# Kernel optimization log

Measured on AMD Instinct MI355X. Metric: run time of the kernel, lower is better.

The kernel has to match this reference:

```python
import jax, jax.numpy as jnp
import numpy as np

EMBED = 1024
ADIM = 1024
H = 16
HD = ADIM // H          # 64
RAY = 48                # ray_subdim
R = RAY // 3            # 16
SCALE = 1.0 / np.sqrt(HD)
NB = 768                # boundary tokens
MN = 8                  # max neighbors
FG = 6                  # face_group
L = 1024                # tokens per face
B = 12                  # b * face_group
STAGES = 4


def _apply_dray(x, d, einsum_str, inverse):
    ray = x[..., :RAY].reshape(x.shape[:-1] + (3, R))
    if inverse:
        d = jnp.swapaxes(d, -1, -2)
    ray = jnp.einsum(einsum_str, d, ray).reshape(x.shape[:-1] + (RAY,))
    return jnp.concatenate([ray, x[..., RAY:]], axis=-1)


def setup_inputs() -> dict:
    key = jax.random.key(0)
    ks = jax.random.split(key, 12)
    inp = {}
    inp['x'] = jax.random.normal(ks[0], (B, L, EMBED), dtype=jnp.float32)
    inp['qkv_w'] = jax.random.normal(ks[1], (EMBED, 3 * ADIM), dtype=jnp.float32) * 0.02
    inp['out_w'] = jax.random.normal(ks[2], (ADIM, EMBED), dtype=jnp.float32) * 0.02
    inp['out_b'] = jax.random.normal(ks[3], (EMBED,), dtype=jnp.float32) * 0.02
    inp['d_ray'] = jax.random.normal(ks[4], (STAGES, FG, L, 3, 3), dtype=jnp.float32)
    inp['boundary_face_ids'] = jax.random.randint(ks[5], (NB,), 0, FG, dtype=jnp.int32).astype(jnp.int64)
    inp['boundary_token_indices'] = jnp.arange(NB, dtype=jnp.int64)
    inp['boundary_local_indices'] = jax.random.randint(ks[6], (NB,), 0, L, dtype=jnp.int32).astype(jnp.int64)
    inp['boundary_stage_ids'] = jax.random.randint(ks[7], (NB,), 0, STAGES, dtype=jnp.int32).astype(jnp.int64)
    inp['neighbor_face_ids'] = jax.random.randint(ks[8], (NB, MN), 0, FG, dtype=jnp.int32).astype(jnp.int64)
    inp['neighbor_token_indices'] = jax.random.randint(ks[9], (NB, MN), 0, L, dtype=jnp.int32).astype(jnp.int64)
    inp['neighbor_local_indices'] = jax.random.randint(ks[10], (NB, MN), 0, L, dtype=jnp.int32).astype(jnp.int64)
    inp['neighbor_stage_ids'] = jax.random.randint(ks[11], (NB, MN), 0, STAGES, dtype=jnp.int32).astype(jnp.int64)
    inp['neighbor_mask'] = jnp.ones((NB, MN), dtype=bool)
    inp['face_group'] = FG
    return inp


def reference(x, qkv_w, out_w, out_b, d_ray,
              boundary_face_ids, boundary_token_indices, boundary_local_indices, boundary_stage_ids,
              neighbor_face_ids, neighbor_token_indices, neighbor_local_indices, neighbor_stage_ids,
              neighbor_mask, face_group):
    b = x.shape[0] // face_group
    l = x.shape[1]
    xt = x.reshape(b, face_group, l, EMBED)          # [b, FG, L, E]
    max_face, max_idx = face_group - 1, l - 1

    qf = jnp.clip(boundary_face_ids, 0, max_face)
    qi = jnp.clip(boundary_token_indices, 0, max_idx)
    valid_q = (boundary_face_ids == qf) & (boundary_token_indices == qi)

    nf = jnp.clip(neighbor_face_ids, 0, max_face)
    ni = jnp.clip(neighbor_token_indices, 0, max_idx)
    mask = neighbor_mask & (neighbor_face_ids == nf) & (neighbor_token_indices == ni)

    # gather boundary queries and neighbor keys/values
    x_q = xt[:, qf, qi, :]                            # [b, NB, E]
    x_kv = xt[:, nf, ni, :]                           # [b, NB, MN, E]
    q = (x_q @ qkv_w)[..., :ADIM]
    kv = x_kv @ qkv_w
    k = kv[..., ADIM:2 * ADIM]
    v = kv[..., 2 * ADIM:]

    nb, mn = q.shape[1], k.shape[2]
    q = q.reshape(b, nb, H, HD)
    k = k.reshape(b, nb, mn, H, HD)
    v = v.reshape(b, nb, mn, H, HD)

    d_q = d_ray[boundary_stage_ids, boundary_face_ids, boundary_local_indices]     # [NB, 3, 3]
    d_k = d_ray[neighbor_stage_ids,
                jnp.maximum(neighbor_face_ids, 0),
                jnp.maximum(neighbor_local_indices, 0)]                            # [NB, MN, 3, 3]

    q = _apply_dray(q, d_q, 'nij,bnhjr->bnhir', inverse=False)
    k = _apply_dray(k, d_k, 'nmij,bnmhjr->bnmhir', inverse=False)
    v = _apply_dray(v, d_k, 'nmij,bnmhjr->bnmhir', inverse=False)

    attn = jnp.einsum('bnhd,bnmhd->bnmh', q, k) * SCALE
    attn = jnp.where(mask[None, :, :, None], attn, -jnp.inf)
    attn = jax.nn.softmax(attn, axis=2)               # softmax over neighbors
    out = jnp.einsum('bnmh,bnmhd->bnhd', attn, v)

    out = _apply_dray(out, d_q, 'nij,bnhjr->bnhir', inverse=True)
    out = out.reshape(b, nb, ADIM) @ out_w + out_b
    out = out * valid_q[None, :, None].astype(out.dtype)

    out_full = jnp.zeros_like(xt).at[:, qf, qi, :].set(out)
    return out_full.reshape(-1, l, EMBED)
```

## Files before the change

kernel.cpp:

```cpp
#include <hip/hip_runtime.h>
#include <hip/hip_bf16.h>
#include <cstddef>

#define FG 6
#define L 1024
#define NB 768
#define MN 8
#define H 16
#define HD 64
#define ADIM 1024
#define STAGES 4
#define SCALE 0.125f

typedef __attribute__((ext_vector_type(8))) short bf16x8;
typedef __attribute__((ext_vector_type(4))) float f32x4;
typedef __attribute__((address_space(3))) short lds_short_t;
typedef const __attribute__((address_space(1))) short g_short_t;

__device__ __forceinline__ int clampi(int v, int lo, int hi) {
  return v < lo ? lo : (v > hi ? hi : v);
}

__device__ __forceinline__ short f2bf(float f) {
  __hip_bfloat16 h = __float2bfloat16(f);
  return *reinterpret_cast<short*>(&h);
}

__device__ __forceinline__ void gload16(const short* g, short* l) {
  __builtin_amdgcn_global_load_lds((g_short_t*)g, (lds_short_t*)l, 16, 0, 0);
}

__global__ __launch_bounds__(256)
void conv_bf16(const float* __restrict__ in, short* __restrict__ out) {
  size_t i = ((size_t)blockIdx.x * 256 + threadIdx.x) * 8;
  float4 a = *(const float4*)(in + i);
  float4 b = *(const float4*)(in + i + 4);
  bf16x8 v;
  v[0] = f2bf(a.x); v[1] = f2bf(a.y); v[2] = f2bf(a.z); v[3] = f2bf(a.w);
  v[4] = f2bf(b.x); v[5] = f2bf(b.y); v[6] = f2bf(b.z); v[7] = f2bf(b.w);
  *(bf16x8*)(out + i) = v;
}

__global__ __launch_bounds__(256)
void transpose_both(const float* __restrict__ qkv_w, short* __restrict__ qwT,
                    const float* __restrict__ out_w, short* __restrict__ owT) {
  const int z = blockIdx.z;
  if (z == 1 && blockIdx.x >= 32) return;
  const float* in = z ? out_w : qkv_w;
  short* out = z ? owT : qwT;
  const int N = z ? 1024 : 3072;
  __shared__ float tile[32][33];
  const int n0 = blockIdx.x * 32, k0 = blockIdx.y * 32;
  const int tx = threadIdx.x & 31, ty = threadIdx.x >> 5;
  #pragma unroll
  for (int i = 0; i < 4; ++i)
    tile[ty + i * 8][tx] = in[(size_t)(k0 + ty + i * 8) * N + n0 + tx];
  __syncthreads();
  #pragma unroll
  for (int i = 0; i < 4; ++i)
    out[(size_t)(n0 + ty + i * 8) * 1024 + k0 + tx] =
        f2bf(tile[tx][ty + i * 8]);
}

__global__ __launch_bounds__(256)
void q_gemm128(const short* __restrict__ A, const short* __restrict__ B,
               float* __restrict__ C,
               const int* __restrict__ f_ids, const int* __restrict__ t_ids)
{
  __shared__ __align__(16) short As[8192];
  __shared__ __align__(16) short Bs[8192];

  const int tid  = threadIdx.x;
  const int w    = tid >> 6, lane = tid & 63;
  const int row0 = blockIdx.y * 128, col0 = blockIdx.x * 128;

  size_t aoff[4], boff[4];
  short *adst[4], *bdst[4];
  #pragma unroll
  for (int c = 0; c < 4; ++c) {
    const int d = (w * 4 + c) * 64 + lane;
    const int r = d >> 3;
    const int ssrc = (d & 7) ^ (r & 7);
    const int rr = row0 + r;
    const int bi = rr >= NB;
    const int idx = rr - bi * NB;
    const int f = clampi(f_ids[idx], 0, FG - 1);
    const int q = clampi(t_ids[idx], 0, L - 1);
    const long gr = (long)(bi * FG + f) * L + q;
    aoff[c] = (size_t)gr * 1024 + ssrc * 8;
    boff[c] = (size_t)(col0 + r) * 1024 + ssrc * 8;
    adst[c] = As + (w * 4 + c) * 512;
    bdst[c] = Bs + (w * 4 + c) * 512;
  }

  const int lr = lane & 15, lq = lane >> 4;
  const int wrow = (w >> 1) * 64, wcol = (w & 1) * 64;
  const int sA = lr & 7;
  const char* As8 = (const char*)As;
  const char* Bs8 = (const char*)Bs;
  const int abase = (wrow + lr) * 128;
  const int bbase = (wcol + lr) * 128;

  f32x4 acc[4][4];
  #pragma unroll
  for (int m = 0; m < 4; ++m)
    #pragma unroll
    for (int n = 0; n < 4; ++n) acc[m][n] = (f32x4){0.f, 0.f, 0.f, 0.f};

  for (int kt = 0; kt < 16; ++kt) {
    #pragma unroll
    for (int c = 0; c < 4; ++c) {
      gload16(A + aoff[c] + kt * 64, adst[c]);
      gload16(B + boff[c] + kt * 64, bdst[c]);
    }
    __syncthreads();
    #pragma unroll
    for (int kk = 0; kk < 2; ++kk) {
      const int so = ((kk * 4 + lq) ^ sA) << 4;
      bf16x8 av[4], bv[4];
      #pragma unroll
      for (int m = 0; m < 4; ++m)
        av[m] = *(const bf16x8*)(As8 + abase + m * 2048 + so);
      #pragma unroll
      for (int n = 0; n < 4; ++n)
        bv[n] = *(const bf16x8*)(Bs8 + bbase + n * 2048 + so);
      #pragma unroll
      for (int m = 0; m < 4; ++m)
        #pragma unroll
        for (int n = 0; n < 4; ++n)
          acc[m][n] = __builtin_amdgcn_mfma_f32_16x16x32_bf16(
              av[m], bv[n], acc[m][n], 0, 0, 0);
    }
    __syncthreads();
  }

  #pragma unroll
  for (int m = 0; m < 4; ++m)
    #pragma unroll
    for (int j = 0; j < 4; ++j) {
      const int r = row0 + wrow + m * 16 + lq * 4 + j;
      #pragma unroll
      for (int n = 0; n < 4; ++n)
        C[(size_t)r * 1024 + col0 + wcol + n * 16 + lr] = acc[m][n][j];
    }
}


#define BAR()   do { __builtin_amdgcn_s_barrier(); __builtin_amdgcn_sched_barrier(0); } while (0)
#define LGKM(N) do { asm volatile("s_waitcnt lgkmcnt(" #N ")" ::: "memory"); __builtin_amdgcn_sched_barrier(0); } while (0)
#define VMC(N)  do { asm volatile("s_waitcnt vmcnt(" #N ")" ::: "memory"); __builtin_amdgcn_sched_barrier(0); } while (0)
#define PRIO1   __builtin_amdgcn_s_setprio(1)
#define PRIO0   __builtin_amdgcn_s_setprio(0)

#define LDA6(D, FB, KK, BUF)                                                  \
  { _Pragma("unroll")                                                         \
    for (int f_ = 0; f_ < 3; ++f_) {                                          \
      const int row_ = (2 * ((FB) + f_) + wm) * 16 + lr;                      \
      D[f_] = *(const bf16x8*)(As8 + (BUF) * 24576 + row_ * 128               \
               + ((((KK) * 4 + lq) ^ swz) << 4));                             \
    } }

#define LDB4(D, KK, BUF)                                                      \
  { _Pragma("unroll")                                                         \
    for (int g_ = 0; g_ < 4; ++g_) {                                          \
      const int row_ = wn * 64 + g_ * 16 + lr;                                \
      D[g_] = *(const bf16x8*)(Bs8 + (BUF) * 32768 + row_ * 128               \
               + ((((KK) * 4 + lq) ^ swz) << 4));                             \
    } }

#define MM6(AV, BV, FB)                                                       \
  { _Pragma("unroll")                                                         \
    for (int f_ = 0; f_ < 3; ++f_)                                            \
      _Pragma("unroll")                                                       \
      for (int g_ = 0; g_ < 4; ++g_)                                          \
        acc[(FB) + f_][g_] = __builtin_amdgcn_mfma_f32_16x16x32_bf16(         \
            AV[f_], BV[g_], acc[(FB) + f_][g_], 0, 0, 0); }

__global__ __launch_bounds__(512, 2)
void kv_gemm192(const short* __restrict__ A, const short* __restrict__ B,
                short* __restrict__ C,
                const int* __restrict__ f_ids, const int* __restrict__ t_ids)
{
  __shared__ __align__(16) short As[24576];
  __shared__ __align__(16) short Bs[32768];

  const int tid = threadIdx.x;
  const int w = tid >> 6, lane = tid & 63;
  const int wm = w >> 2, wn = w & 3;
  const int lr = lane & 15, lq = lane >> 4;
  const int row0 = blockIdx.y * 192;
  const int col0 = blockIdx.x * 256;

  const int ssrc = (((tid & 7) ^ ((tid >> 3) & 7))) * 8;

  size_t a_src[3];
  #pragma unroll
  for (int c = 0; c < 3; ++c) {
    const int rr = row0 + c * 64 + (tid >> 3);
    const int bi = rr >= NB * MN;
    const int idx = rr - bi * (NB * MN);
    const int f = clampi(f_ids[idx], 0, FG - 1);
    const int q = clampi(t_ids[idx], 0, L - 1);
    a_src[c] = (size_t)((bi * FG + f) * L + q) * 1024 + ssrc;
  }
  size_t b_src[2][2];
  #pragma unroll
  for (int h = 0; h < 2; ++h)
    #pragma unroll
    for (int i = 0; i < 2; ++i)
      b_src[h][i] = (size_t)(1024 + col0 + h * 128 + ((tid + i * 512) >> 3)) * 1024 + ssrc;

  auto stgA = [&](int c, int kt, int buf) {
    gload16(A + a_src[c] + kt * 64, As + buf * 12288 + c * 4096 + tid * 8);
  };
  auto stgB = [&](int h, int kt, int buf) {
    gload16(B + b_src[h][0] + kt * 64, Bs + buf * 16384 + h * 8192 + tid * 8);
    gload16(B + b_src[h][1] + kt * 64, Bs + buf * 16384 + h * 8192 + 4096 + tid * 8);
  };

  const char* As8 = (const char*)As;
  const char* Bs8 = (const char*)Bs;
  const int swz = lane & 7;

  f32x4 acc[6][4];
  #pragma unroll
  for (int f = 0; f < 6; ++f)
    #pragma unroll
    for (int g = 0; g < 4; ++g) acc[f][g] = (f32x4){0.f, 0.f, 0.f, 0.f};

  bf16x8 avA[3], avB[3], bv0[4], bv1[4];

  stgB(0, 0, 0); stgB(1, 0, 0); stgA(0, 0, 0); stgA(1, 0, 0); stgA(2, 0, 0);
  stgB(0, 1, 1); stgB(1, 1, 1); stgA(0, 1, 1);
  VMC(5); BAR();
  LDA6(avA, 0, 0, 0); LDB4(bv0, 0, 0);

  for (int I = 0; I < 7; ++I) {
    const int kA = 2 * I + 1, kB = 2 * I + 2, kC = 2 * I + 3;
    BAR(); stgA(1, kA, 1);
    LDA6(avB, 0, 1, 0); LDB4(bv1, 1, 0);
    LGKM(7); PRIO1; MM6(avA, bv0, 0); PRIO0;
    BAR(); stgA(2, kA, 1);
    LDA6(avA, 3, 0, 0);
    LGKM(3); PRIO1; MM6(avB, bv1, 0); PRIO0;
    BAR(); stgB(0, kB, 0); VMC(2);
    LDA6(avB, 3, 1, 0);
    LGKM(3); PRIO1; MM6(avA, bv0, 3); PRIO0;
    BAR(); stgB(1, kB, 0); stgA(0, kB, 0);
    LDA6(avA, 0, 0, 1); LDB4(bv0, 0, 1);
    LGKM(7); PRIO1; MM6(avB, bv1, 3); PRIO0;
    BAR(); stgA(1, kB, 0);
    LDA6(avB, 0, 1, 1); LDB4(bv1, 1, 1);
    LGKM(7); PRIO1; MM6(avA, bv0, 0); PRIO0;
    BAR(); stgA(2, kB, 0);
    LDA6(avA, 3, 0, 1);
    LGKM(3); PRIO1; MM6(avB, bv1, 0); PRIO0;
    BAR(); stgB(0, kC, 1); VMC(2);
    LDA6(avB, 3, 1, 1);
    LGKM(3); PRIO1; MM6(avA, bv0, 3); PRIO0;
    BAR(); stgB(1, kC, 1); stgA(0, kC, 1);
    LDA6(avA, 0, 0, 0); LDB4(bv0, 0, 0);
    LGKM(7); PRIO1; MM6(avB, bv1, 3); PRIO0;
  }

  {
    BAR(); stgA(1, 15, 1);
    LDA6(avB, 0, 1, 0); LDB4(bv1, 1, 0);
    LGKM(7); PRIO1; MM6(avA, bv0, 0); PRIO0;

    BAR(); stgA(2, 15, 1);
    LDA6(avA, 3, 0, 0);
    LGKM(3); PRIO1; MM6(avB, bv1, 0); PRIO0;

    BAR(); VMC(0);
    LDA6(avB, 3, 1, 0);
    LGKM(3); PRIO1; MM6(avA, bv0, 3); PRIO0;

    BAR();
    LDA6(avA, 0, 0, 1); LDB4(bv0, 0, 1);
    LGKM(7); PRIO1; MM6(avB, bv1, 3); PRIO0;

    BAR();
    LDA6(avB, 0, 1, 1); LDB4(bv1, 1, 1);
    LGKM(7); PRIO1; MM6(avA, bv0, 0); PRIO0;

    BAR();
    LDA6(avA, 3, 0, 1);
    LGKM(3); PRIO1; MM6(avB, bv1, 0); PRIO0;

    BAR();
    LDA6(avB, 3, 1, 1);
    LGKM(3); PRIO1; MM6(avA, bv0, 3); PRIO0;

    BAR();
    LGKM(0); PRIO1; MM6(avB, bv1, 3); PRIO0;
  }

  #pragma unroll
  for (int f = 0; f < 6; ++f) {
    #pragma unroll
    for (int j = 0; j < 4; ++j) {
      const int r = row0 + (2 * f + wm) * 16 + lq * 4 + j;
      short* cp = C + (size_t)r * 2048 + col0 + wn * 64 + lr;
      #pragma unroll
      for (int g = 0; g < 4; ++g)
        cp[g * 16] = f2bf(acc[f][g][j]);
    }
  }
}

__global__ __launch_bounds__(256)
void out_gemm64(const short* __restrict__ A, const short* __restrict__ B,
                float* __restrict__ C,
                const int* __restrict__ f_ids, const int* __restrict__ t_ids,
                const float* __restrict__ bias)
{
  __shared__ __align__(16) short As[4096];
  __shared__ __align__(16) short Bs[8192];

  const int tid = threadIdx.x;
  const int w = tid >> 6, lane = tid & 63;
  const int row0 = blockIdx.y * 64, col0 = blockIdx.x * 128;
  const int lr = lane & 15, lq = lane >> 4;
  const int wrow = (w >> 1) * 32, wcol = (w & 1) * 64;

  size_t asrc[2]; short* adst[2];
  #pragma unroll
  for (int c = 0; c < 2; ++c) {
    const int d = c * 256 + tid, r = d >> 3;
    const int ss = (d & 7) ^ (r & 7);
    asrc[c] = (size_t)(row0 + r) * 1024 + ss * 8;
    adst[c] = As + d * 8;
  }
  size_t bsrc[4]; short* bdst[4];
  #pragma unroll
  for (int c = 0; c < 4; ++c) {
    const int d = c * 256 + tid, r = d >> 3;
    const int ss = (d & 7) ^ (r & 7);
    bsrc[c] = (size_t)(col0 + r) * 1024 + ss * 8;
    bdst[c] = Bs + d * 8;
  }

  const char* As8 = (const char*)As;
  const char* Bs8 = (const char*)Bs;
  const int swz = lr & 7;

  f32x4 acc[2][4];
  #pragma unroll
  for (int m = 0; m < 2; ++m)
    #pragma unroll
    for (int n = 0; n < 4; ++n) acc[m][n] = (f32x4){0.f, 0.f, 0.f, 0.f};

  for (int kt = 0; kt < 16; ++kt) {
    #pragma unroll
    for (int c = 0; c < 2; ++c) gload16(A + asrc[c] + kt * 64, adst[c]);
    #pragma unroll
    for (int c = 0; c < 4; ++c) gload16(B + bsrc[c] + kt * 64, bdst[c]);
    __syncthreads();
    #pragma unroll
    for (int kk = 0; kk < 2; ++kk) {
      const int so = ((kk * 4 + lq) ^ swz) << 4;
      bf16x8 av[2], bv[4];
      #pragma unroll
      for (int m = 0; m < 2; ++m)
        av[m] = *(const bf16x8*)(As8 + (wrow + m * 16 + lr) * 128 + so);
      #pragma unroll
      for (int n = 0; n < 4; ++n)
        bv[n] = *(const bf16x8*)(Bs8 + (wcol + n * 16 + lr) * 128 + so);
      #pragma unroll
      for (int m = 0; m < 2; ++m)
        #pragma unroll
        for (int n = 0; n < 4; ++n)
          acc[m][n] = __builtin_amdgcn_mfma_f32_16x16x32_bf16(
              av[m], bv[n], acc[m][n], 0, 0, 0);
    }
    __syncthreads();
  }

  float bb[4];
  #pragma unroll
  for (int n = 0; n < 4; ++n) bb[n] = bias[col0 + wcol + n * 16 + lr];
  #pragma unroll
  for (int m = 0; m < 2; ++m)
    #pragma unroll
    for (int j = 0; j < 4; ++j) {
      const int r  = row0 + wrow + m * 16 + lq * 4 + j;
      const int bi = r >= NB;
      const int nn = r - bi * NB;
      const int bf = f_ids[nn], bt = t_ids[nn];
      const int qf = clampi(bf, 0, FG - 1), qi = clampi(bt, 0, L - 1);
      const bool valid = (bf == qf) && (bt == qi);
      const size_t obase = ((size_t)(bi * FG + qf) * L + qi) * 1024;
      #pragma unroll
      for (int n = 0; n < 4; ++n) {
        const int col = col0 + wcol + n * 16 + lr;
        C[obase + col] = valid ? (acc[m][n][j] + bb[n]) : 0.f;
      }
    }
}

__global__ __launch_bounds__(256)
void attn_kernel(const float* __restrict__ dray,
                 const int* __restrict__ bfid, const int* __restrict__ blid,
                 const int* __restrict__ bsid,
                 const int* __restrict__ nfid, const int* __restrict__ ntid,
                 const int* __restrict__ nlid, const int* __restrict__ nsid,
                 const int* __restrict__ nmask,
                 const float* __restrict__ qbuf,
                 const __hip_bfloat16* __restrict__ kvbuf,
                 __hip_bfloat16* __restrict__ obuf)
{
  const int lane = threadIdx.x & 63;
  const int gw   = blockIdx.x * 4 + (threadIdx.x >> 6);
  const int h    = gw & (H - 1);
  const int bn   = gw >> 4;
  const int n    = bn % NB;

  int st = clampi(bsid[n], 0, STAGES - 1);
  int f  = clampi(bfid[n], 0, FG - 1);
  int lc = clampi(blid[n], 0, L - 1);
  const float* dqp = dray + ((size_t)(st * FG + f) * L + lc) * 9;
  float dq[9];
  #pragma unroll
  for (int t = 0; t < 9; ++t) dq[t] = dqp[t];

  const float qraw = qbuf[(size_t)bn * ADIM + h * HD + lane];
  const int rr = lane & 15;

  float x0 = __shfl(qraw, rr), x1 = __shfl(qraw, 16 + rr), x2 = __shfl(qraw, 32 + rr);
  float q0 = dq[0]*x0 + dq[1]*x1 + dq[2]*x2;
  float q1 = dq[3]*x0 + dq[4]*x1 + dq[5]*x2;
  float q2 = dq[6]*x0 + dq[7]*x1 + dq[8]*x2;
  float qd = lane < 16 ? q0 : lane < 32 ? q1 : lane < 48 ? q2 : qraw;

  const __hip_bfloat16* kvb = kvbuf + (size_t)bn * MN * 2048 + h * HD;
  float s[MN], vd[MN];
  #pragma unroll
  for (int m = 0; m < MN; ++m) {
    const int idx = n * MN + m;
    int nst = clampi(nsid[idx], 0, STAGES - 1);
    int nfc = clampi(nfid[idx], 0, FG - 1);
    int nlc = clampi(nlid[idx], 0, L - 1);
    const float* dkp = dray + ((size_t)(nst * FG + nfc) * L + nlc) * 9;
    float dk[9];
    #pragma unroll
    for (int t = 0; t < 9; ++t) dk[t] = dkp[t];

    float kraw = __bfloat162float(kvb[(size_t)m * 2048 + lane]);
    float k0 = __shfl(kraw, rr), k1 = __shfl(kraw, 16 + rr), k2 = __shfl(kraw, 32 + rr);
    float kr0 = dk[0]*k0 + dk[1]*k1 + dk[2]*k2;
    float kr1 = dk[3]*k0 + dk[4]*k1 + dk[5]*k2;
    float kr2 = dk[6]*k0 + dk[7]*k1 + dk[8]*k2;
    float kd = lane < 16 ? kr0 : lane < 32 ? kr1 : lane < 48 ? kr2 : kraw;

    float p = qd * kd;
    #pragma unroll
    for (int off = 32; off; off >>= 1) p += __shfl_xor(p, off);
    s[m] = p;

    float vraw = __bfloat162float(kvb[(size_t)m * 2048 + 1024 + lane]);
    float v0 = __shfl(vraw, rr), v1 = __shfl(vraw, 16 + rr), v2 = __shfl(vraw, 32 + rr);
    float vr0 = dk[0]*v0 + dk[1]*v1 + dk[2]*v2;
    float vr1 = dk[3]*v0 + dk[4]*v1 + dk[5]*v2;
    float vr2 = dk[6]*v0 + dk[7]*v1 + dk[8]*v2;
    vd[m] = lane < 16 ? vr0 : lane < 32 ? vr1 : lane < 48 ? vr2 : vraw;
  }

  float mx = -INFINITY;
  #pragma unroll
  for (int m = 0; m < MN; ++m) {
    const int idx = n * MN + m;
    int nf = nfid[idx], nt = ntid[idx];
    bool ok = (nmask[idx] != 0) && nf >= 0 && nf < FG && nt >= 0 && nt < L;
    s[m] = ok ? s[m] * SCALE : -INFINITY;
    mx = fmaxf(mx, s[m]);
  }
  float den = 0.f;
  #pragma unroll
  for (int m = 0; m < MN; ++m) { s[m] = expf(s[m] - mx); den += s[m]; }
  float inv = 1.0f / den;

  float od = 0.f;
  #pragma unroll
  for (int m = 0; m < MN; ++m) od += s[m] * vd[m];
  od *= inv;

  float y0 = __shfl(od, rr), y1 = __shfl(od, 16 + rr), y2 = __shfl(od, 32 + rr);
  float t0 = dq[0]*y0 + dq[3]*y1 + dq[6]*y2;
  float t1 = dq[1]*y0 + dq[4]*y1 + dq[7]*y2;
  float t2 = dq[2]*y0 + dq[5]*y1 + dq[8]*y2;
  float outd = lane < 16 ? t0 : lane < 32 ? t1 : lane < 48 ? t2 : od;

  obuf[(size_t)bn * ADIM + h * HD + lane] = __float2bfloat16(outd);
}

extern "C" void kernel_launch(void* const* d_in, const int* in_sizes, int n_in,
                              void* d_out, int out_size, void* d_ws, size_t ws_size,
                              hipStream_t stream) {
  const float* x     = (const float*)d_in[0];
  const float* qkv_w = (const float*)d_in[1];
  const float* out_w = (const float*)d_in[2];
  const float* out_b = (const float*)d_in[3];
  const float* dray  = (const float*)d_in[4];
  const int* bfid  = (const int*)d_in[5];
  const int* btid  = (const int*)d_in[6];
  const int* blid  = (const int*)d_in[7];
  const int* bsid  = (const int*)d_in[8];
  const int* nfid  = (const int*)d_in[9];
  const int* ntid  = (const int*)d_in[10];
  const int* nlid  = (const int*)d_in[11];
  const int* nsid  = (const int*)d_in[12];
  const int* nmask = (const int*)d_in[13];

  char* ws = (char*)d_ws;
  short* xb    = (short*)(ws);
  short* qwT   = (short*)(ws + 25165824);
  short* owT   = (short*)(ws + 31457280);
  float* qbuf  = (float*)(ws + 33554432);
  short* kvbuf = (short*)(ws + 39845888);
  short* obuf  = (short*)(ws + 90177536);

  (void)hipMemsetAsync(d_out, 0, (size_t)out_size * sizeof(float), stream);

  conv_bf16<<<6144, 256, 0, stream>>>(x, xb);
  transpose_both<<<dim3(96, 32, 2), 256, 0, stream>>>(qkv_w, qwT, out_w, owT);

  q_gemm128<<<dim3(8, 12), 256, 0, stream>>>(xb, qwT, qbuf, bfid, btid);
  kv_gemm192<<<dim3(8, 64), 512, 0, stream>>>(xb, qwT, kvbuf, nfid, ntid);
  attn_kernel<<<6144, 256, 0, stream>>>(dray, bfid, blid, bsid,
                                        nfid, ntid, nlid, nsid, nmask,
                                        qbuf, (const __hip_bfloat16*)kvbuf,
                                        (__hip_bfloat16*)obuf);
  out_gemm64<<<dim3(8, 24), 256, 0, stream>>>(obuf, owT, (float*)d_out,
                                              bfid, btid, out_b);
}
```

Before: 176.4 us.

## Shrink Q GEMM row tile to 64 and restructure KV GEMM pipeline barriers

The Q projection GEMM now uses a 64x128 tile instead of 128x128 and launches twice as many blocks (8x24 instead of 8x12), to fill more compute units on a small problem. Separately, the KV GEMM main loop is reordered so every MFMA phase is enclosed by barriers with a full LDS wait (lgkmcnt 0). The earlier software pipeline, which overlapped LDS reads of the next fragment with the current MFMAs, is removed. This may simplify correctness, but it costs overlap between LDS reads and matrix math in the larger KV GEMM.

Result: faster. 165.7 us (-6.1%).

```diff
diff --git a/kernel.cpp b/kernel.cpp
--- a/kernel.cpp
+++ b/kernel.cpp
@@ -63,69 +63,69 @@
 }
 
 __global__ __launch_bounds__(256)
-void q_gemm128(const short* __restrict__ A, const short* __restrict__ B,
-               float* __restrict__ C,
-               const int* __restrict__ f_ids, const int* __restrict__ t_ids)
+void q_gemm64(const short* __restrict__ A, const short* __restrict__ B,
+              float* __restrict__ C,
+              const int* __restrict__ f_ids, const int* __restrict__ t_ids)
 {
-  __shared__ __align__(16) short As[8192];
+  __shared__ __align__(16) short As[4096];
   __shared__ __align__(16) short Bs[8192];
 
-  const int tid  = threadIdx.x;
-  const int w    = tid >> 6, lane = tid & 63;
-  const int row0 = blockIdx.y * 128, col0 = blockIdx.x * 128;
-
-  size_t aoff[4], boff[4];
-  short *adst[4], *bdst[4];
-  #pragma unroll
-  for (int c = 0; c < 4; ++c) {
-    const int d = (w * 4 + c) * 64 + lane;
-    const int r = d >> 3;
-    const int ssrc = (d & 7) ^ (r & 7);
+  const int tid = threadIdx.x;
+  const int w = tid >> 6, lane = tid & 63;
+  const int row0 = blockIdx.y * 64, col0 = blockIdx.x * 128;
+  const int lr = lane & 15, lq = lane >> 4;
+  const int wrow = (w >> 1) * 32, wcol = (w & 1) * 64;
+
+  size_t asrc[2]; short* adst[2];
+  #pragma unroll
+  for (int c = 0; c < 2; ++c) {
+    const int d = c * 256 + tid, r = d >> 3;
+    const int ss = (d & 7) ^ (r & 7);
     const int rr = row0 + r;
     const int bi = rr >= NB;
     const int idx = rr - bi * NB;
     const int f = clampi(f_ids[idx], 0, FG - 1);
     const int q = clampi(t_ids[idx], 0, L - 1);
-    const long gr = (long)(bi * FG + f) * L + q;
-    aoff[c] = (size_t)gr * 1024 + ssrc * 8;
-    boff[c] = (size_t)(col0 + r) * 1024 + ssrc * 8;
-    adst[c] = As + (w * 4 + c) * 512;
-    bdst[c] = Bs + (w * 4 + c) * 512;
-  }
-
-  const int lr = lane & 15, lq = lane >> 4;
-  const int wrow = (w >> 1) * 64, wcol = (w & 1) * 64;
-  const int sA = lr & 7;
+    asrc[c] = (size_t)((bi * FG + f) * L + q) * 1024 + ss * 8;
+    adst[c] = As + d * 8;
+  }
+  size_t bsrc[4]; short* bdst[4];
+  #pragma unroll
+  for (int c = 0; c < 4; ++c) {
+    const int d = c * 256 + tid, r = d >> 3;
+    const int ss = (d & 7) ^ (r & 7);
+    bsrc[c] = (size_t)(col0 + r) * 1024 + ss * 8;
+    bdst[c] = Bs + d * 8;
+  }
+
   const char* As8 = (const char*)As;
   const char* Bs8 = (const char*)Bs;
-  const int abase = (wrow + lr) * 128;
-  const int bbase = (wcol + lr) * 128;
-
-  f32x4 acc[4][4];
-  #pragma unroll
-  for (int m = 0; m < 4; ++m)
+  const int swz = lr & 7;
+
+  f32x4 acc[2][4];
+  #pragma unroll
+  for (int m = 0; m < 2; ++m)
     #pragma unroll
     for (int n = 0; n < 4; ++n) acc[m][n] = (f32x4){0.f, 0.f, 0.f, 0.f};
 
   for (int kt = 0; kt < 16; ++kt) {
     #pragma unroll
-    for (int c = 0; c < 4; ++c) {
-      gload16(A + aoff[c] + kt * 64, adst[c]);
-      gload16(B + boff[c] + kt * 64, bdst[c]);
-    }
+    for (int c = 0; c < 2; ++c) gload16(A + asrc[c] + kt * 64, adst[c]);
+    #pragma unroll
+    for (int c = 0; c < 4; ++c) gload16(B + bsrc[c] + kt * 64, bdst[c]);
     __syncthreads();
     #pragma unroll
     for (int kk = 0; kk < 2; ++kk) {
-      const int so = ((kk * 4 + lq) ^ sA) << 4;
-      bf16x8 av[4], bv[4];
-      #pragma unroll
-      for (int m = 0; m < 4; ++m)
-        av[m] = *(const bf16x8*)(As8 + abase + m * 2048 + so);
+      const int so = ((kk * 4 + lq) ^ swz) << 4;
+      bf16x8 av[2], bv[4];
+      #pragma unroll
+      for (int m = 0; m < 2; ++m)
+        av[m] = *(const bf16x8*)(As8 + (wrow + m * 16 + lr) * 128 + so);
       #pragma unroll
       for (int n = 0; n < 4; ++n)
-        bv[n] = *(const bf16x8*)(Bs8 + bbase + n * 2048 + so);
-      #pragma unroll
-      for (int m = 0; m < 4; ++m)
+        bv[n] = *(const bf16x8*)(Bs8 + (wcol + n * 16 + lr) * 128 + so);
+      #pragma unroll
+      for (int m = 0; m < 2; ++m)
         #pragma unroll
         for (int n = 0; n < 4; ++n)
           acc[m][n] = __builtin_amdgcn_mfma_f32_16x16x32_bf16(
@@ -135,7 +135,7 @@
   }
 
   #pragma unroll
-  for (int m = 0; m < 4; ++m)
+  for (int m = 0; m < 2; ++m)
     #pragma unroll
     for (int j = 0; j < 4; ++j) {
       const int r = row0 + wrow + m * 16 + lq * 4 + j;
@@ -233,67 +233,51 @@
   stgB(0, 0, 0); stgB(1, 0, 0); stgA(0, 0, 0); stgA(1, 0, 0); stgA(2, 0, 0);
   stgB(0, 1, 1); stgB(1, 1, 1); stgA(0, 1, 1);
   VMC(5); BAR();
-  LDA6(avA, 0, 0, 0); LDB4(bv0, 0, 0);
 
   for (int I = 0; I < 7; ++I) {
     const int kA = 2 * I + 1, kB = 2 * I + 2, kC = 2 * I + 3;
-    BAR(); stgA(1, kA, 1);
-    LDA6(avB, 0, 1, 0); LDB4(bv1, 1, 0);
-    LGKM(7); PRIO1; MM6(avA, bv0, 0); PRIO0;
-    BAR(); stgA(2, kA, 1);
+    LDA6(avA, 0, 0, 0); LDB4(bv0, 0, 0); stgA(1, kA, 1);
+    BAR(); LGKM(0); PRIO1; MM6(avA, bv0, 0); PRIO0; BAR();
+    LDA6(avB, 0, 1, 0); LDB4(bv1, 1, 0); stgA(2, kA, 1);
+    BAR(); LGKM(0); PRIO1; MM6(avB, bv1, 0); PRIO0; BAR();
+    LDA6(avA, 3, 0, 0); stgB(0, kB, 0);
+    BAR(); LGKM(0); PRIO1; MM6(avA, bv0, 3); PRIO0; BAR();
+    LDA6(avB, 3, 1, 0); stgB(1, kB, 0); stgA(0, kB, 0);
+    BAR(); LGKM(0); PRIO1; MM6(avB, bv1, 3); PRIO0; VMC(5); BAR();
+    LDA6(avA, 0, 0, 1); LDB4(bv0, 0, 1); stgA(1, kB, 0);
+    BAR(); LGKM(0); PRIO1; MM6(avA, bv0, 0); PRIO0; BAR();
+    LDA6(avB, 0, 1, 1); LDB4(bv1, 1, 1); stgA(2, kB, 0);
+    BAR(); LGKM(0); PRIO1; MM6(avB, bv1, 0); PRIO0; BAR();
+    LDA6(avA, 3, 0, 1); stgB(0, kC, 1);
+    BAR(); LGKM(0); PRIO1; MM6(avA, bv0, 3); PRIO0; BAR();
+    LDA6(avB, 3, 1, 1); stgB(1, kC, 1); stgA(0, kC, 1);
+    BAR(); LGKM(0); PRIO1; MM6(avB, bv1, 3); PRIO0; VMC(5); BAR();
+  }
+
+  {
+    LDA6(avA, 0, 0, 0); LDB4(bv0, 0, 0); stgA(1, 15, 1);
+    BAR(); LGKM(0); PRIO1; MM6(avA, bv0, 0); PRIO0; BAR();
+
+    LDA6(avB, 0, 1, 0); LDB4(bv1, 1, 0); stgA(2, 15, 1);
+    BAR(); LGKM(0); PRIO1; MM6(avB, bv1, 0); PRIO0; BAR();
+
     LDA6(avA, 3, 0, 0);
-    LGKM(3); PRIO1; MM6(avB, bv1, 0); PRIO0;
-    BAR(); stgB(0, kB, 0); VMC(2);
+    BAR(); LGKM(0); PRIO1; MM6(avA, bv0, 3); PRIO0; BAR();
+
     LDA6(avB, 3, 1, 0);
-    LGKM(3); PRIO1; MM6(avA, bv0, 3); PRIO0;
-    BAR(); stgB(1, kB, 0); stgA(0, kB, 0);
+    BAR(); LGKM(0); PRIO1; MM6(avB, bv1, 3); PRIO0; VMC(0); BAR();
+
     LDA6(avA, 0, 0, 1); LDB4(bv0, 0, 1);
-    LGKM(7); PRIO1; MM6(avB, bv1, 3); PRIO0;
-    BAR(); stgA(1, kB, 0);
+    BAR(); LGKM(0); PRIO1; MM6(avA, bv0, 0); PRIO0; BAR();
+
     LDA6(avB, 0, 1, 1); LDB4(bv1, 1, 1);
-    LGKM(7); PRIO1; MM6(avA, bv0, 0); PRIO0;
-    BAR(); stgA(2, kB, 0);
+    BAR(); LGKM(0); PRIO1; MM6(avB, bv1, 0); PRIO0; BAR();
+
     LDA6(avA, 3, 0, 1);
-    LGKM(3); PRIO1; MM6(avB, bv1, 0); PRIO0;
-    BAR(); stgB(0, kC, 1); VMC(2);
+    BAR(); LGKM(0); PRIO1; MM6(avA, bv0, 3); PRIO0; BAR();
+
     LDA6(avB, 3, 1, 1);
-    LGKM(3); PRIO1; MM6(avA, bv0, 3); PRIO0;
-    BAR(); stgB(1, kC, 1); stgA(0, kC, 1);
-    LDA6(avA, 0, 0, 0); LDB4(bv0, 0, 0);
-    LGKM(7); PRIO1; MM6(avB, bv1, 3); PRIO0;
-  }
-
-  {
-    BAR(); stgA(1, 15, 1);
-    LDA6(avB, 0, 1, 0); LDB4(bv1, 1, 0);
-    LGKM(7); PRIO1; MM6(avA, bv0, 0); PRIO0;
-
-    BAR(); stgA(2, 15, 1);
-    LDA6(avA, 3, 0, 0);
-    LGKM(3); PRIO1; MM6(avB, bv1, 0); PRIO0;
-
-    BAR(); VMC(0);
-    LDA6(avB, 3, 1, 0);
-    LGKM(3); PRIO1; MM6(avA, bv0, 3); PRIO0;
-
-    BAR();
-    LDA6(avA, 0, 0, 1); LDB4(bv0, 0, 1);
-    LGKM(7); PRIO1; MM6(avB, bv1, 3); PRIO0;
-
-    BAR();
-    LDA6(avB, 0, 1, 1); LDB4(bv1, 1, 1);
-    LGKM(7); PRIO1; MM6(avA, bv0, 0); PRIO0;
-
-    BAR();
-    LDA6(avA, 3, 0, 1);
-    LGKM(3); PRIO1; MM6(avB, bv1, 0); PRIO0;
-
-    BAR();
-    LDA6(avB, 3, 1, 1);
-    LGKM(3); PRIO1; MM6(avA, bv0, 3); PRIO0;
-
-    BAR();
-    LGKM(0); PRIO1; MM6(avB, bv1, 3); PRIO0;
+    BAR(); LGKM(0); PRIO1; MM6(avB, bv1, 3); PRIO0;
   }
 
   #pragma unroll
@@ -525,7 +509,7 @@
   conv_bf16<<<6144, 256, 0, stream>>>(x, xb);
   transpose_both<<<dim3(96, 32, 2), 256, 0, stream>>>(qkv_w, qwT, out_w, owT);
 
-  q_gemm128<<<dim3(8, 12), 256, 0, stream>>>(xb, qwT, qbuf, bfid, btid);
+  q_gemm64<<<dim3(8, 24), 256, 0, stream>>>(xb, qwT, qbuf, bfid, btid);
   kv_gemm192<<<dim3(8, 64), 512, 0, stream>>>(xb, qwT, kvbuf, nfid, ntid);
   attn_kernel<<<6144, 256, 0, stream>>>(dray, bfid, blid, bsid,
                                         nfid, ntid, nlid, nsid, nmask,
```
